# Optimization experiments

Hardware: AMD Instinct MI355X
Metric: run time of the kernel (lower is better)

## Reference

```python
import jax, jax.numpy as jnp
import numpy as np
from jax import lax

DIM = 384
HEADS = 8
DS = 2  # down_scale


def setup_inputs() -> dict:
    key = jax.random.key(0)
    ks = jax.random.split(key, 6)
    d = DIM
    x = jax.random.normal(ks[0], (1, d, 192, 192), jnp.float32)
    w_qkv = jax.random.normal(ks[1], (3 * d, d), jnp.float32) * 0.02   # 1x1 conv dim->3dim
    b_qkv = jnp.zeros((3 * d,), jnp.float32)
    w_dw = jax.random.normal(ks[2], (3 * d, 1, 3, 3), jnp.float32) * 0.1  # depthwise 3x3
    b_dw = jnp.zeros((3 * d,), jnp.float32)
    w_proj = jax.random.normal(ks[3], (d, d), jnp.float32) * 0.02      # 1x1 conv dim->dim
    b_proj = jnp.zeros((d,), jnp.float32)
    temperature = jnp.ones((HEADS, 1, 1), jnp.float32)
    a1 = jnp.array([0.2], jnp.float32)
    a2 = jnp.array([0.2], jnp.float32)
    a3 = jnp.array([0.2], jnp.float32)
    a4 = jnp.array([0.2], jnp.float32)
    return {"x": x, "w_qkv": w_qkv, "b_qkv": b_qkv, "w_dw": w_dw, "b_dw": b_dw,
            "w_proj": w_proj, "b_proj": b_proj, "temperature": temperature,
            "a1": a1, "a2": a2, "a3": a3, "a4": a4}


def _topk_softmax(attn, kk):
    # exact scatter semantics of torch: mask=1 at top-k indices along last dim
    idx = lax.top_k(attn, kk)[1]                                   # [b,h,C,kk]
    mask = jax.nn.one_hot(idx, attn.shape[-1], dtype=attn.dtype).sum(-2)  # [b,h,C,C]
    return jax.nn.softmax(jnp.where(mask > 0, attn, -jnp.inf), axis=-1)


def reference(x, w_qkv, b_qkv, w_dw, b_dw, w_proj, b_proj, temperature, a1, a2, a3, a4):
    b, c, h, w = x.shape
    # 1x1 qkv conv
    qkv = jnp.einsum('bchw,oc->bohw', x, w_qkv) + b_qkv[None, :, None, None]
    # adaptive_max_pool2d to (h//DS, w//DS) == strided max pool since h,w % DS == 0
    hs, ws = h // DS, w // DS
    qkv = qkv.reshape(b, 3 * c, hs, DS, ws, DS).max(axis=(3, 5))
    # 3x3 depthwise conv, padding=1
    qkv = lax.conv_general_dilated(qkv, w_dw, (1, 1), 'SAME',
                                   feature_group_count=3 * c,
                                   dimension_numbers=('NCHW', 'OIHW', 'NCHW'))
    qkv = qkv + b_dw[None, :, None, None]
    q, k, v = jnp.split(qkv, 3, axis=1)
    hw = hs * ws
    C = c // HEADS
    q = q.reshape(b, HEADS, C, hw)
    k = k.reshape(b, HEADS, C, hw)
    v = v.reshape(b, HEADS, C, hw)
    # L2 normalize along spatial dim (F.normalize, eps=1e-12)
    q = q / jnp.clip(jnp.linalg.norm(q, axis=-1, keepdims=True), 1e-12)
    k = k / jnp.clip(jnp.linalg.norm(k, axis=-1, keepdims=True), 1e-12)
    # channel attention: [b,h,C,C]
    attn = jnp.einsum('bhcn,bhdn->bhcd', q, k) * temperature[None]
    out = (_topk_softmax(attn, C // 2) @ v) * a1 \
        + (_topk_softmax(attn, C * 2 // 3) @ v) * a2 \
        + (_topk_softmax(attn, C * 3 // 4) @ v) * a3 \
        + (_topk_softmax(attn, C * 4 // 5) @ v) * a4
    out = out.reshape(b, c, hs, ws)
    out = jax.nn.gelu(out, approximate=False)  # nn.GELU() exact erf form
    # nearest-neighbor upsample back to (h, w) == repeat by DS (exact since h = DS*hs)
    out = jnp.repeat(jnp.repeat(out, DS, axis=2), DS, axis=3)
    out = jnp.einsum('bchw,oc->bohw', out, w_proj) + b_proj[None, :, None, None]
    return out
```

## Files before the change

kernel.cpp:

```cpp
#include <hip/hip_runtime.h>
#include <hip/hip_bf16.h>
#include <math.h>

#define NH    8
#define CPH   48
#define D     384
#define QC    1152
#define HF    192
#define WFULL 192
#define HP    96
#define WP    96
#define NP    9216
#define NF    36864

typedef __attribute__((ext_vector_type(8))) short short8;
typedef __attribute__((ext_vector_type(4))) float f32x4;

__device__ __forceinline__ float gelu_exact(float v) {
    return 0.5f * v * (1.f + erff(v * 0.70710678118654752440f));
}
__device__ __forceinline__ ushort f2bf(float v) {
    __hip_bfloat16 h = __float2bfloat16(v);
    return *reinterpret_cast<ushort*>(&h);
}
__device__ __forceinline__ float bf2f(ushort u) {
    __hip_bfloat16 h = *reinterpret_cast<__hip_bfloat16*>(&u);
    return __bfloat162float(h);
}

__global__ __launch_bounds__(256) void k_prep_w(
    const float* __restrict__ w, ushort* __restrict__ wh, ushort* __restrict__ wl, int n) {
    int i = blockIdx.x * 256 + threadIdx.x;
    if (i < n) {
        float v = w[i];
        ushort h = f2bf(v);
        wh[i] = h;
        wl[i] = f2bf(v - bf2f(h));
    }
}

__global__ __launch_bounds__(256) void k_prep(
    const float* __restrict__ wq, ushort* __restrict__ wh, ushort* __restrict__ wl,
    const float* __restrict__ x, ushort* __restrict__ xh, ushort* __restrict__ xl) {
    __shared__ float xf[64][128];
    const int tid = threadIdx.x;
    if (blockIdx.x < 1728) {
        int i = blockIdx.x * 256 + tid;
        float v = wq[i];
        ushort h = f2bf(v);
        wh[i] = h;
        wl[i] = f2bf(v - bf2f(h));
        return;
    }
    const int e  = blockIdx.x - 1728;
    const int xt = e % 288, kt = e / 288;
    const int kk = kt * 64;
    const int q0 = xt * 32;
    const int py = q0 / 96, px0 = q0 - py * 96;
    const int y0 = 2 * py, xcol0 = 2 * px0;
    const float* xb = x + (size_t)kk * NF + (size_t)y0 * WFULL + xcol0;
#pragma unroll
    for (int it = 0; it < 8; it++) {
        int li = tid + 256 * it;
        int ch = li >> 5, r = (li >> 4) & 1, c4 = (li & 15) * 4;
        float4 v = *(const float4*)&xb[(size_t)ch * NF + r * WFULL + c4];
        *(float4*)&xf[ch][r * 64 + c4] = v;
    }
    __syncthreads();
    const int row = tid >> 1, half = tid & 1;
    const int r = (row >> 1) & 1;
    const int col = (row >> 2) * 2 + (row & 1);
    const int src = r * 64 + col;
    const size_t np = (size_t)xt * 128 + row;
    ushort hbuf[32], lbuf[32];
#pragma unroll
    for (int j = 0; j < 32; j++) {
        float v = xf[half * 32 + j][src];
        ushort h = f2bf(v);
        hbuf[j] = h;
        lbuf[j] = f2bf(v - bf2f(h));
    }
    ushort* dh = xh + np * D + kk + half * 32;
    ushort* dl = xl + np * D + kk + half * 32;
#pragma unroll
    for (int j = 0; j < 4; j++) {
        *(short8*)&dh[j * 8] = *(const short8*)&hbuf[j * 8];
        *(short8*)&dl[j * 8] = *(const short8*)&lbuf[j * 8];
    }
}

__global__ __launch_bounds__(512) void k_qkv_mfma(
    const ushort* __restrict__ xh, const ushort* __restrict__ xl,
    const ushort* __restrict__ wh, const ushort* __restrict__ wl,
    const float* __restrict__ bq, float* __restrict__ pooled) {
    __shared__ ushort lds[2][4][4096];
    const int tid = threadIdx.x;
    const int lane = tid & 63, wid = tid >> 6;
    const int wm = wid >> 2, wn = wid & 3;

    const int d   = blockIdx.x;
    const int xcd = d & 7;
    const int idx = d >> 3;
    const int by  = xcd * 36 + idx / 9;
    const int bx  = idx % 9;
    const int n0 = bx * 128;
    const int m0 = by * 128;

    const ushort* srcs[4];
    srcs[0] = xh + (size_t)m0 * D;
    srcs[1] = xl + (size_t)m0 * D;
    srcs[2] = wh + (size_t)n0 * D;
    srcs[3] = wl + (size_t)n0 * D;

    f32x4 acc[4][2];
#pragma unroll
    for (int i = 0; i < 4; i++)
#pragma unroll
        for (int j = 0; j < 2; j++) acc[i][j] = (f32x4){0.f, 0.f, 0.f, 0.f};

    int a_off[4], b_off[2];
#pragma unroll
    for (int f = 0; f < 4; f++) {
        int ra = wm * 64 + f * 16 + (lane & 15);
        a_off[f] = ra * 64 + ((((lane >> 4) ^ ((ra >> 1) & 3)) & 3) << 4);
    }
#pragma unroll
    for (int f = 0; f < 2; f++) {
        int rb = wn * 32 + f * 16 + (lane & 15);
        b_off[f] = rb * 64 + ((((lane >> 4) ^ ((rb >> 1) & 3)) & 3) << 4);
    }

    auto STAGE = [&](int buf, int kk) {
#pragma unroll
        for (int i = 0; i < 4; i++) {
            const int row = wid * 16 + (lane >> 2);
            const int scol = (((lane & 3) ^ ((row >> 1) & 3)) & 3) << 4;
            const ushort* src = srcs[i] + (size_t)row * D + kk + (scol >> 1);
            __builtin_amdgcn_global_load_lds(
                (const __attribute__((address_space(1))) void*)src,
                (__attribute__((address_space(3))) void*)&lds[buf][i][wid * 512],
                16, 0, 0);
        }
    };

    STAGE(0, 0);
    for (int t = 0; t < 12; ++t) {
        const int cur = t & 1;
        asm volatile("s_waitcnt vmcnt(0)" ::: "memory");
        __builtin_amdgcn_s_barrier();
        if (t < 11) STAGE(cur ^ 1, (t + 1) * 32);

        const char* bA0 = (const char*)&lds[cur][0][0];
        const char* bA1 = (const char*)&lds[cur][1][0];
        const char* bB0 = (const char*)&lds[cur][2][0];
        const char* bB1 = (const char*)&lds[cur][3][0];
        short8 A[2][4], B[2][2];
#pragma unroll
        for (int f = 0; f < 4; f++) {
            A[0][f] = *(const short8*)(bA0 + a_off[f]);
            A[1][f] = *(const short8*)(bA1 + a_off[f]);
        }
#pragma unroll
        for (int f = 0; f < 2; f++) {
            B[0][f] = *(const short8*)(bB0 + b_off[f]);
            B[1][f] = *(const short8*)(bB1 + b_off[f]);
        }
        __builtin_amdgcn_s_setprio(1);
#pragma unroll
        for (int fm = 0; fm < 4; fm++)
#pragma unroll
            for (int fn = 0; fn < 2; fn++) {
                acc[fm][fn] = __builtin_amdgcn_mfma_f32_16x16x32_bf16(A[0][fm], B[0][fn], acc[fm][fn], 0, 0, 0);
                acc[fm][fn] = __builtin_amdgcn_mfma_f32_16x16x32_bf16(A[0][fm], B[1][fn], acc[fm][fn], 0, 0, 0);
                acc[fm][fn] = __builtin_amdgcn_mfma_f32_16x16x32_bf16(A[1][fm], B[0][fn], acc[fm][fn], 0, 0, 0);
            }
        __builtin_amdgcn_s_setprio(0);
    }

    const int p_base = by * 32 + wm * 16 + (lane >> 4);
#pragma unroll
    for (int fn = 0; fn < 2; fn++) {
        const int o = n0 + wn * 32 + fn * 16 + (lane & 15);
        const float b = bq[o];
#pragma unroll
        for (int fm = 0; fm < 4; fm++) {
            f32x4 v = acc[fm][fn];
            float mx = fmaxf(fmaxf(v.x, v.y), fmaxf(v.z, v.w)) + b;
            pooled[(size_t)o * NP + p_base + fm * 4] = mx;
        }
    }
}

__global__ __launch_bounds__(256) void k_dwconv(
    const float* __restrict__ pooled, const float* __restrict__ wd,
    const float* __restrict__ bd, float* __restrict__ out) {
    int gid = blockIdx.x * 256 + threadIdx.x;
    int xq = gid % 24, t = gid / 24;
    int y = t % 96, ch = t / 96;
    const float* src = pooled + (size_t)ch * NP;
    const float* w = wd + ch * 9;
    const int x0 = xq * 4;
    float b = bd[ch];
    float o0 = b, o1 = b, o2 = b, o3 = b;
#pragma unroll
    for (int dy = 0; dy < 3; dy++) {
        int yy = y + dy - 1;
        if (yy < 0 || yy >= HP) continue;
        const float* r = src + yy * WP;
        float4 c = *(const float4*)&r[x0];
        float lm = (x0 > 0) ? r[x0 - 1] : 0.f;
        float rm = (x0 < 92) ? r[x0 + 4] : 0.f;
        float w0 = w[dy * 3], w1 = w[dy * 3 + 1], w2 = w[dy * 3 + 2];
        o0 += w0 * lm  + w1 * c.x + w2 * c.y;
        o1 += w0 * c.x + w1 * c.y + w2 * c.z;
        o2 += w0 * c.y + w1 * c.z + w2 * c.w;
        o3 += w0 * c.z + w1 * c.w + w2 * rm;
    }
    *(float4*)&out[(size_t)ch * NP + y * WP + x0] = make_float4(o0, o1, o2, o3);
}

__global__ __launch_bounds__(256) void k_attn_part(
    const float* __restrict__ qkv, float* __restrict__ Spart,
    float* __restrict__ qnpart, float* __restrict__ knpart) {
    __shared__ float qs[48][196], ks[48][196];
    const int tid = threadIdx.x;
    const int p = blockIdx.x, h = blockIdx.y;
    const int n0 = p * 192;
    const float* qb = qkv + (size_t)(h * CPH) * NP + n0;
    const float* kb = qkv + (size_t)(D + h * CPH) * NP + n0;
#pragma unroll
    for (int it = 0; it < 9; it++) {
        int li = tid + 256 * it;
        int row = li / 48, c4 = (li - row * 48) * 4;
        *(float4*)&qs[row][c4] = *(const float4*)&qb[(size_t)row * NP + c4];
        *(float4*)&ks[row][c4] = *(const float4*)&kb[(size_t)row * NP + c4];
    }
    __syncthreads();
    const int tr = (tid >> 4) * 3, tc = (tid & 15) * 3;
    float acc[3][3] = {};
    for (int n = 0; n < 192; n++) {
        float qv[3], kv[3];
#pragma unroll
        for (int i = 0; i < 3; i++) qv[i] = qs[tr + i][n];
#pragma unroll
        for (int j = 0; j < 3; j++) kv[j] = ks[tc + j][n];
#pragma unroll
        for (int i = 0; i < 3; i++)
#pragma unroll
            for (int j = 0; j < 3; j++) acc[i][j] += qv[i] * kv[j];
    }
    float* Sp = Spart + (size_t)(p * NH + h) * 2304;
#pragma unroll
    for (int i = 0; i < 3; i++)
#pragma unroll
        for (int j = 0; j < 3; j++)
            Sp[(tr + i) * CPH + tc + j] = acc[i][j];
    if (tid < 48) {
        float s = 0.f;
        for (int n = 0; n < 192; n++) s += qs[tid][n] * qs[tid][n];
        qnpart[(p * NH + h) * CPH + tid] = s;
    } else if (tid >= 64 && tid < 112) {
        int t2 = tid - 64;
        float s = 0.f;
        for (int n = 0; n < 192; n++) s += ks[t2][n] * ks[t2][n];
        knpart[(p * NH + h) * CPH + t2] = s;
    }
}

__global__ __launch_bounds__(256) void k_softmax(
    const float* __restrict__ Spart, const float* __restrict__ qnpart,
    const float* __restrict__ knpart, const float* __restrict__ temp,
    const float* __restrict__ a1, const float* __restrict__ a2,
    const float* __restrict__ a3, const float* __restrict__ a4,
    float* __restrict__ Wc) {
    __shared__ float rowbuf[4][64];
    int lane = threadIdx.x & 63;
    int w = threadIdx.x >> 6;
    int row = blockIdx.x * 4 + w;
    int h = row / CPH, c = row % CPH;
    float a = -INFINITY;
    if (lane < CPH) {
        float s = 0.f, q2 = 0.f, k2 = 0.f;
        for (int p = 0; p < 48; p++) {
            int base = (p * NH + h);
            s  += Spart[(size_t)base * 2304 + c * CPH + lane];
            q2 += qnpart[base * CPH + c];
            k2 += knpart[base * CPH + lane];
        }
        float nq = fmaxf(sqrtf(fmaxf(q2, 0.f)), 1e-12f);
        float nk = fmaxf(sqrtf(fmaxf(k2, 0.f)), 1e-12f);
        a = s / (nq * nk) * temp[h];
    }
    rowbuf[w][lane] = a;
    __syncthreads();
    int rank = 0;
    float m = -INFINITY;
    for (int j = 0; j < CPH; j++) {
        float vj = rowbuf[w][j];
        m = fmaxf(m, vj);
        rank += (vj > a || (vj == a && j < lane)) ? 1 : 0;
    }
    float e = (lane < CPH) ? expf(a - m) : 0.f;
    float4 p;
    p.x = (rank < 24) ? e : 0.f;
    p.y = (rank < 32) ? e : 0.f;
    p.z = (rank < 36) ? e : 0.f;
    p.w = (rank < 38) ? e : 0.f;
#pragma unroll
    for (int off = 32; off > 0; off >>= 1) {
        p.x += __shfl_xor(p.x, off);
        p.y += __shfl_xor(p.y, off);
        p.z += __shfl_xor(p.z, off);
        p.w += __shfl_xor(p.w, off);
    }
    if (lane < CPH) {
        float wv = 0.f;
        if (rank < 24) wv += a1[0] / p.x;
        if (rank < 32) wv += a2[0] / p.y;
        if (rank < 36) wv += a3[0] / p.z;
        if (rank < 38) wv += a4[0] / p.w;
        Wc[(h * CPH + c) * CPH + lane] = e * wv;
    }
}

__global__ __launch_bounds__(256) void k_av_gelu(
    const float* __restrict__ qkv, const float* __restrict__ Wc,
    ushort* __restrict__ o96h, ushort* __restrict__ o96l) {
    __shared__ float Ws[48][16];
    __shared__ float vs[48][256];
    const int tid = threadIdx.x;
    const int b = blockIdx.x;
    const int h = b / 108;
    const int rem = b - h * 108;
    const int t3 = rem / 36;
    const int pc = rem - t3 * 36;
    const int c0 = t3 * 16;
    const int px0 = pc * 256;
    for (int li = tid; li < 768; li += 256) {
        int dd = li >> 4, cc = li & 15;
        Ws[dd][cc] = Wc[(h * CPH + c0 + cc) * CPH + dd];
    }
    const float* vb = qkv + (size_t)(2 * D + h * CPH) * NP + px0;
#pragma unroll
    for (int it = 0; it < 12; it++) {
        int li = tid + 256 * it;
        int dd = li >> 6, c4 = (li & 63) * 4;
        *(float4*)&vs[dd][c4] = *(const float4*)&vb[(size_t)dd * NP + c4];
    }
    __syncthreads();
    float acc[16] = {};
#pragma unroll 4
    for (int dd = 0; dd < 48; dd++) {
        float vv = vs[dd][tid];
        float4 w0 = *(const float4*)&Ws[dd][0];
        float4 w1 = *(const float4*)&Ws[dd][4];
        float4 w2 = *(const float4*)&Ws[dd][8];
        float4 w3 = *(const float4*)&Ws[dd][12];
        acc[0]  += w0.x * vv; acc[1]  += w0.y * vv; acc[2]  += w0.z * vv; acc[3]  += w0.w * vv;
        acc[4]  += w1.x * vv; acc[5]  += w1.y * vv; acc[6]  += w1.z * vv; acc[7]  += w1.w * vv;
        acc[8]  += w2.x * vv; acc[9]  += w2.y * vv; acc[10] += w2.z * vv; acc[11] += w2.w * vv;
        acc[12] += w3.x * vv; acc[13] += w3.y * vv; acc[14] += w3.z * vv; acc[15] += w3.w * vv;
    }
    short8 hv0, hv1, lv0, lv1;
#pragma unroll
    for (int j = 0; j < 8; j++) {
        float g = gelu_exact(acc[j]);
        ushort hu = f2bf(g);
        hv0[j] = (short)hu; lv0[j] = (short)f2bf(g - bf2f(hu));
        float g2 = gelu_exact(acc[8 + j]);
        ushort hu2 = f2bf(g2);
        hv1[j] = (short)hu2; lv1[j] = (short)f2bf(g2 - bf2f(hu2));
    }
    size_t base = (size_t)(px0 + tid) * D + h * CPH + c0;
    *(short8*)&o96h[base] = hv0;
    *(short8*)&o96h[base + 8] = hv1;
    *(short8*)&o96l[base] = lv0;
    *(short8*)&o96l[base + 8] = lv1;
}

__global__ __launch_bounds__(256) void k_proj_mfma(
    const ushort* __restrict__ wph, const ushort* __restrict__ wpl,
    const ushort* __restrict__ o96h, const ushort* __restrict__ o96l,
    const float* __restrict__ bp, float* __restrict__ out) {
    __shared__ ushort lds[2][4][4096];
    const int tid = threadIdx.x;
    const int lane = tid & 63, wid = tid >> 6;
    const int wm = wid >> 1, wn = wid & 1;

    const int d   = blockIdx.x;
    const int xcd = d & 7;
    const int idx = d >> 3;
    const int nt  = xcd * 9 + idx / 3;
    const int ot  = idx % 3;
    const int o0 = ot * 128;
    const int n0 = nt * 128;

    const ushort* srcs[4];
    srcs[0] = wph + (size_t)o0 * D;
    srcs[1] = wpl + (size_t)o0 * D;
    srcs[2] = o96h + (size_t)n0 * D;
    srcs[3] = o96l + (size_t)n0 * D;

    f32x4 acc[4][4];
#pragma unroll
    for (int i = 0; i < 4; i++)
#pragma unroll
        for (int j = 0; j < 4; j++) acc[i][j] = (f32x4){0.f, 0.f, 0.f, 0.f};

    int a_off[4], b_off[4];
#pragma unroll
    for (int f = 0; f < 4; f++) {
        int ra = wm * 64 + f * 16 + (lane & 15);
        a_off[f] = ra * 64 + ((((lane >> 4) ^ ((ra >> 1) & 3)) & 3) << 4);
        int rb = wn * 64 + f * 16 + (lane & 15);
        b_off[f] = rb * 64 + ((((lane >> 4) ^ ((rb >> 1) & 3)) & 3) << 4);
    }

    auto STAGE = [&](int buf, int kk) {
#pragma unroll
        for (int i = 0; i < 8; i++) {
            const int mat = i >> 1;
            const int cm  = ((i & 1) << 2) | wid;
            const int row = cm * 16 + (lane >> 2);
            const int scol = (((lane & 3) ^ ((row >> 1) & 3)) & 3) << 4;
            const ushort* src = srcs[mat] + (size_t)row * D + kk + (scol >> 1);
            __builtin_amdgcn_global_load_lds(
                (const __attribute__((address_space(1))) void*)src,
                (__attribute__((address_space(3))) void*)&lds[buf][mat][cm * 512],
                16, 0, 0);
        }
    };

    STAGE(0, 0);
    for (int t = 0; t < 12; ++t) {
        const int cur = t & 1;
        asm volatile("s_waitcnt vmcnt(0)" ::: "memory");
        __builtin_amdgcn_s_barrier();
        if (t < 11) STAGE(cur ^ 1, (t + 1) * 32);

        const char* bA0 = (const char*)&lds[cur][0][0];
        const char* bA1 = (const char*)&lds[cur][1][0];
        const char* bB0 = (const char*)&lds[cur][2][0];
        const char* bB1 = (const char*)&lds[cur][3][0];
        short8 A[2][4], B[2][4];
#pragma unroll
        for (int f = 0; f < 4; f++) {
            A[0][f] = *(const short8*)(bA0 + a_off[f]);
            A[1][f] = *(const short8*)(bA1 + a_off[f]);
            B[0][f] = *(const short8*)(bB0 + b_off[f]);
            B[1][f] = *(const short8*)(bB1 + b_off[f]);
        }
        __builtin_amdgcn_s_setprio(1);
#pragma unroll
        for (int fm = 0; fm < 4; fm++)
#pragma unroll
            for (int fn = 0; fn < 4; fn++) {
                acc[fm][fn] = __builtin_amdgcn_mfma_f32_16x16x32_bf16(A[0][fm], B[0][fn], acc[fm][fn], 0, 0, 0);
                acc[fm][fn] = __builtin_amdgcn_mfma_f32_16x16x32_bf16(A[0][fm], B[1][fn], acc[fm][fn], 0, 0, 0);
                acc[fm][fn] = __builtin_amdgcn_mfma_f32_16x16x32_bf16(A[1][fm], B[0][fn], acc[fm][fn], 0, 0, 0);
            }
        __builtin_amdgcn_s_setprio(0);
    }

#pragma unroll
    for (int fn = 0; fn < 4; fn++) {
        const int n = n0 + wn * 64 + fn * 16 + (lane & 15);
        const int y = n / WP, xcol = n - y * WP;
        const size_t pbase = (size_t)(2 * y) * WFULL + 2 * xcol;
#pragma unroll
        for (int fm = 0; fm < 4; fm++) {
            f32x4 v = acc[fm][fn];
#pragma unroll
            for (int j = 0; j < 4; j++) {
                const int o = o0 + wm * 64 + fm * 16 + (lane >> 4) * 4 + j;
                const float val = v[j] + bp[o];
                float2 vv = make_float2(val, val);
                size_t base = (size_t)o * NF + pbase;
                *(float2*)&out[base] = vv;
                *(float2*)&out[base + WFULL] = vv;
            }
        }
    }
}

extern "C" void kernel_launch(void* const* d_in, const int* in_sizes, int n_in,
                              void* d_out, int out_size, void* d_ws, size_t ws_size,
                              hipStream_t stream) {
    (void)in_sizes; (void)n_in; (void)out_size; (void)ws_size;
    const float* x    = (const float*)d_in[0];
    const float* wq   = (const float*)d_in[1];
    const float* bq   = (const float*)d_in[2];
    const float* wd   = (const float*)d_in[3];
    const float* bd   = (const float*)d_in[4];
    const float* wp   = (const float*)d_in[5];
    const float* bp   = (const float*)d_in[6];
    const float* temp = (const float*)d_in[7];
    const float* a1   = (const float*)d_in[8];
    const float* a2   = (const float*)d_in[9];
    const float* a3   = (const float*)d_in[10];
    const float* a4   = (const float*)d_in[11];
    float* out = (float*)d_out;
    float* ws  = (float*)d_ws;

    float* pooled = ws;
    float* Wc     = ws + 10616832;
    ushort* wh    = (ushort*)(Wc + 18432 + 19200);
    ushort* wl    = wh + 442368;

    ushort* o96h   = (ushort*)ws;
    ushort* o96l   = o96h + 3538944;
    float*  Spart  = (float*)((char*)ws + 14155776);
    float*  qnpart = Spart + 884736;
    float*  knpart = qnpart + 18432;
    ushort* wph    = (ushort*)(knpart + 18432);
    ushort* wpl    = wph + 147456;

    float* qkvdw = out;
    ushort* xh = (ushort*)d_out;
    ushort* xl = xh + 14155776;

    hipLaunchKernelGGL(k_prep,      dim3(3456),    dim3(256), 0, stream, wq, wh, wl, x, xh, xl);
    hipLaunchKernelGGL(k_qkv_mfma,  dim3(2592),    dim3(512), 0, stream, xh, xl, wh, wl, bq, pooled);
    hipLaunchKernelGGL(k_dwconv,    dim3(10368),   dim3(256), 0, stream, pooled, wd, bd, qkvdw);
    hipLaunchKernelGGL(k_prep_w,    dim3(576),     dim3(256), 0, stream, wp, wph, wpl, D * D);
    hipLaunchKernelGGL(k_attn_part, dim3(48, 8),   dim3(256), 0, stream, qkvdw, Spart, qnpart, knpart);
    hipLaunchKernelGGL(k_softmax,   dim3(96),      dim3(256), 0, stream, Spart, qnpart, knpart, temp, a1, a2, a3, a4, Wc);
    hipLaunchKernelGGL(k_av_gelu,   dim3(864),     dim3(256), 0, stream, qkvdw, Wc, o96h, o96l);
    hipLaunchKernelGGL(k_proj_mfma, dim3(216),     dim3(256), 0, stream, wph, wpl, o96h, o96l, bp, out);
}
```

Baseline: 215.1 us.

## Pad prep LDS tile, single-buffer qkv GEMM, reuse V tile across channel groups

Pads the k_prep shared tile rows from 128 to 132 floats to avoid LDS bank conflicts during the transpose. Switches the qkv MFMA GEMM from a double-buffered LDS pipeline to a single buffer with an extra barrier per k-step. This halves LDS use, probably to raise occupancy, but gives up the overlap of global loads with MFMA work. Merges the three channel-group blocks of k_av_gelu into one block that loads the V tile once and loops over the groups. This cuts redundant V reads but leaves only 288 blocks.

```diff
diff --git a/kernel.cpp b/kernel.cpp
--- a/kernel.cpp
+++ b/kernel.cpp
@@ -42,7 +42,7 @@
 __global__ __launch_bounds__(256) void k_prep(
     const float* __restrict__ wq, ushort* __restrict__ wh, ushort* __restrict__ wl,
     const float* __restrict__ x, ushort* __restrict__ xh, ushort* __restrict__ xl) {
-    __shared__ float xf[64][128];
+    __shared__ float xf[64][132];
     const int tid = threadIdx.x;
     if (blockIdx.x < 1728) {
         int i = blockIdx.x * 256 + tid;
@@ -93,7 +93,7 @@
     const ushort* __restrict__ xh, const ushort* __restrict__ xl,
     const ushort* __restrict__ wh, const ushort* __restrict__ wl,
     const float* __restrict__ bq, float* __restrict__ pooled) {
-    __shared__ ushort lds[2][4][4096];
+    __shared__ ushort lds[4][4096];
     const int tid = threadIdx.x;
     const int lane = tid & 63, wid = tid >> 6;
     const int wm = wid >> 2, wn = wid & 3;
@@ -130,7 +130,7 @@
         b_off[f] = rb * 64 + ((((lane >> 4) ^ ((rb >> 1) & 3)) & 3) << 4);
     }
 
-    auto STAGE = [&](int buf, int kk) {
+    auto STAGE = [&](int kk) {
 #pragma unroll
         for (int i = 0; i < 4; i++) {
             const int row = wid * 16 + (lane >> 2);
@@ -138,22 +138,20 @@
             const ushort* src = srcs[i] + (size_t)row * D + kk + (scol >> 1);
             __builtin_amdgcn_global_load_lds(
                 (const __attribute__((address_space(1))) void*)src,
-                (__attribute__((address_space(3))) void*)&lds[buf][i][wid * 512],
+                (__attribute__((address_space(3))) void*)&lds[i][wid * 512],
                 16, 0, 0);
         }
     };
 
-    STAGE(0, 0);
     for (int t = 0; t < 12; ++t) {
-        const int cur = t & 1;
+        STAGE(t * 32);
         asm volatile("s_waitcnt vmcnt(0)" ::: "memory");
         __builtin_amdgcn_s_barrier();
-        if (t < 11) STAGE(cur ^ 1, (t + 1) * 32);
-
-        const char* bA0 = (const char*)&lds[cur][0][0];
-        const char* bA1 = (const char*)&lds[cur][1][0];
-        const char* bB0 = (const char*)&lds[cur][2][0];
-        const char* bB1 = (const char*)&lds[cur][3][0];
+
+        const char* bA0 = (const char*)&lds[0][0];
+        const char* bA1 = (const char*)&lds[1][0];
+        const char* bB0 = (const char*)&lds[2][0];
+        const char* bB1 = (const char*)&lds[3][0];
         short8 A[2][4], B[2][2];
 #pragma unroll
         for (int f = 0; f < 4; f++) {
@@ -175,6 +173,7 @@
                 acc[fm][fn] = __builtin_amdgcn_mfma_f32_16x16x32_bf16(A[1][fm], B[0][fn], acc[fm][fn], 0, 0, 0);
             }
         __builtin_amdgcn_s_setprio(0);
+        if (t < 11) __builtin_amdgcn_s_barrier();
     }
 
     const int p_base = by * 32 + wm * 16 + (lane >> 4);
@@ -326,19 +325,17 @@
 __global__ __launch_bounds__(256) void k_av_gelu(
     const float* __restrict__ qkv, const float* __restrict__ Wc,
     ushort* __restrict__ o96h, ushort* __restrict__ o96l) {
-    __shared__ float Ws[48][16];
+    __shared__ float Ws[3][48][16];
     __shared__ float vs[48][256];
     const int tid = threadIdx.x;
     const int b = blockIdx.x;
-    const int h = b / 108;
-    const int rem = b - h * 108;
-    const int t3 = rem / 36;
-    const int pc = rem - t3 * 36;
-    const int c0 = t3 * 16;
+    const int h = b / 36;
+    const int pc = b - h * 36;
     const int px0 = pc * 256;
-    for (int li = tid; li < 768; li += 256) {
-        int dd = li >> 4, cc = li & 15;
-        Ws[dd][cc] = Wc[(h * CPH + c0 + cc) * CPH + dd];
+    for (int li = tid; li < 2304; li += 256) {
+        int t3 = li / 768, r = li - t3 * 768;
+        int dd = r >> 4, cc = r & 15;
+        Ws[t3][dd][cc] = Wc[(h * CPH + t3 * 16 + cc) * CPH + dd];
     }
     const float* vb = qkv + (size_t)(2 * D + h * CPH) * NP + px0;
 #pragma unroll
@@ -348,34 +345,36 @@
         *(float4*)&vs[dd][c4] = *(const float4*)&vb[(size_t)dd * NP + c4];
     }
     __syncthreads();
-    float acc[16] = {};
+    for (int t3 = 0; t3 < 3; t3++) {
+        float acc[16] = {};
 #pragma unroll 4
-    for (int dd = 0; dd < 48; dd++) {
-        float vv = vs[dd][tid];
-        float4 w0 = *(const float4*)&Ws[dd][0];
-        float4 w1 = *(const float4*)&Ws[dd][4];
-        float4 w2 = *(const float4*)&Ws[dd][8];
-        float4 w3 = *(const float4*)&Ws[dd][12];
-        acc[0]  += w0.x * vv; acc[1]  += w0.y * vv; acc[2]  += w0.z * vv; acc[3]  += w0.w * vv;
-        acc[4]  += w1.x * vv; acc[5]  += w1.y * vv; acc[6]  += w1.z * vv; acc[7]  += w1.w * vv;
-        acc[8]  += w2.x * vv; acc[9]  += w2.y * vv; acc[10] += w2.z * vv; acc[11] += w2.w * vv;
-        acc[12] += w3.x * vv; acc[13] += w3.y * vv; acc[14] += w3.z * vv; acc[15] += w3.w * vv;
-    }
-    short8 hv0, hv1, lv0, lv1;
-#pragma unroll
-    for (int j = 0; j < 8; j++) {
-        float g = gelu_exact(acc[j]);
-        ushort hu = f2bf(g);
-        hv0[j] = (short)hu; lv0[j] = (short)f2bf(g - bf2f(hu));
-        float g2 = gelu_exact(acc[8 + j]);
-        ushort hu2 = f2bf(g2);
-        hv1[j] = (short)hu2; lv1[j] = (short)f2bf(g2 - bf2f(hu2));
-    }
-    size_t base = (size_t)(px0 + tid) * D + h * CPH + c0;
-    *(short8*)&o96h[base] = hv0;
-    *(short8*)&o96h[base + 8] = hv1;
-    *(short8*)&o96l[base] = lv0;
-    *(short8*)&o96l[base + 8] = lv1;
+        for (int dd = 0; dd < 48; dd++) {
+            float vv = vs[dd][tid];
+            float4 w0 = *(const float4*)&Ws[t3][dd][0];
+            float4 w1 = *(const float4*)&Ws[t3][dd][4];
+            float4 w2 = *(const float4*)&Ws[t3][dd][8];
+            float4 w3 = *(const float4*)&Ws[t3][dd][12];
+            acc[0]  += w0.x * vv; acc[1]  += w0.y * vv; acc[2]  += w0.z * vv; acc[3]  += w0.w * vv;
+            acc[4]  += w1.x * vv; acc[5]  += w1.y * vv; acc[6]  += w1.z * vv; acc[7]  += w1.w * vv;
+            acc[8]  += w2.x * vv; acc[9]  += w2.y * vv; acc[10] += w2.z * vv; acc[11] += w2.w * vv;
+            acc[12] += w3.x * vv; acc[13] += w3.y * vv; acc[14] += w3.z * vv; acc[15] += w3.w * vv;
+        }
+        short8 hv0, hv1, lv0, lv1;
+#pragma unroll
+        for (int j = 0; j < 8; j++) {
+            float g = gelu_exact(acc[j]);
+            ushort hu = f2bf(g);
+            hv0[j] = (short)hu; lv0[j] = (short)f2bf(g - bf2f(hu));
+            float g2 = gelu_exact(acc[8 + j]);
+            ushort hu2 = f2bf(g2);
+            hv1[j] = (short)hu2; lv1[j] = (short)f2bf(g2 - bf2f(hu2));
+        }
+        size_t base = (size_t)(px0 + tid) * D + h * CPH + t3 * 16;
+        *(short8*)&o96h[base] = hv0;
+        *(short8*)&o96h[base + 8] = hv1;
+        *(short8*)&o96l[base] = lv0;
+        *(short8*)&o96l[base + 8] = lv1;
+    }
 }
 
 __global__ __launch_bounds__(256) void k_proj_mfma(
@@ -525,6 +524,6 @@
     hipLaunchKernelGGL(k_prep_w,    dim3(576),     dim3(256), 0, stream, wp, wph, wpl, D * D);
     hipLaunchKernelGGL(k_attn_part, dim3(48, 8),   dim3(256), 0, stream, qkvdw, Spart, qnpart, knpart);
     hipLaunchKernelGGL(k_softmax,   dim3(96),      dim3(256), 0, stream, Spart, qnpart, knpart, temp, a1, a2, a3, a4, Wc);
-    hipLaunchKernelGGL(k_av_gelu,   dim3(864),     dim3(256), 0, stream, qkvdw, Wc, o96h, o96l);
+    hipLaunchKernelGGL(k_av_gelu,   dim3(288),     dim3(256), 0, stream, qkvdw, Wc, o96h, o96l);
     hipLaunchKernelGGL(k_proj_mfma, dim3(216),     dim3(256), 0, stream, wph, wpl, o96h, o96l, bp, out);
 }
```

Measured after the change: 231.6 us. 1.08x slower.
